# Performance work log

Measured on AMD Instinct MI355X. Metric: run time of the kernel, lower is better.

Reference implementation:

```python
import jax, jax.numpy as jnp
import numpy as np

N, D_MODEL, D_FFN, K = 8192, 1024, 4096, 512


def setup_inputs() -> dict:
    key = jax.random.key(0)
    ks = jax.random.split(key, 5)
    x = jax.random.normal(ks[0], (N, D_MODEL), dtype=jnp.float32)
    topk_indices = jax.random.randint(ks[1], (N, K), 0, D_FFN, dtype=jnp.int32)
    scale = 0.02
    w_gate = jax.random.normal(ks[2], (D_MODEL, D_FFN), dtype=jnp.float32) * scale
    w_up = jax.random.normal(ks[3], (D_MODEL, D_FFN), dtype=jnp.float32) * scale
    w_down = jax.random.normal(ks[4], (D_FFN, D_MODEL), dtype=jnp.float32) * scale
    return {"x": x, "topk_indices": topk_indices, "w_gate": w_gate, "w_up": w_up, "w_down": w_down}


def reference(x, topk_indices, w_gate, w_up, w_down):
    # Dense gate/up projections: [N, d_ffn]
    G = x @ w_gate
    U = x @ w_up
    # Gather only the top-k active neurons per token and fuse SwiGLU there.
    G_act = jnp.take_along_axis(G, topk_indices, axis=1)  # [N, k]
    U_act = jnp.take_along_axis(U, topk_indices, axis=1)  # [N, k]
    Z_active = jax.nn.silu(G_act) * U_act                 # [N, k]
    # Sparse-to-dense down projection: scatter active activations back into
    # the d_ffn axis (zeros elsewhere), then dense matmul with w_down.
    n, k = topk_indices.shape
    rows = jnp.arange(n, dtype=topk_indices.dtype)[:, None]
    Z_dense = jnp.zeros((n, w_down.shape[0]), dtype=Z_active.dtype).at[rows, topk_indices].add(Z_active)
    return Z_dense @ w_down  # [N, d_model]
```

## Files before the change

### kernel.cpp

```cpp
#include <hip/hip_runtime.h>
#include <hip/hip_bf16.h>
#include <cstdint>
#include <cstddef>

#define N_TOK   8192
#define D_MODEL 1024
#define D_FFN   4096
#define K_TOP   512
#define NHALF   2048

typedef __bf16 bf16_t;
typedef __bf16 bf16x8 __attribute__((ext_vector_type(8)));
typedef __bf16 bf16x4 __attribute__((ext_vector_type(4)));
typedef float  f32x4  __attribute__((ext_vector_type(4)));


__global__ void cvt_f32_bf16(const float* __restrict__ in, bf16_t* __restrict__ out, int n4) {
  int i = blockIdx.x * blockDim.x + threadIdx.x;
  if (i < n4) {
    const f32x4 v = ((const f32x4*)in)[i];
    bf16x4 o;
    o[0] = (bf16_t)v[0]; o[1] = (bf16_t)v[1]; o[2] = (bf16_t)v[2]; o[3] = (bf16_t)v[3];
    ((bf16x4*)out)[i] = o;
  }
}

__global__ void transpose_cvt(const float* __restrict__ in, bf16_t* __restrict__ out,
                              int rows, int cols) {
  __shared__ float tile[32][33];
  const int tx = threadIdx.x, ty = threadIdx.y;
  const int x = blockIdx.x * 32 + tx;
#pragma unroll
  for (int i = 0; i < 32; i += 8) {
    int y = blockIdx.y * 32 + ty + i;
    tile[ty + i][tx] = in[(size_t)y * cols + x];
  }
  __syncthreads();
  const int xo = blockIdx.y * 32 + tx;
#pragma unroll
  for (int i = 0; i < 32; i += 8) {
    int yo = blockIdx.x * 32 + ty + i;
    out[(size_t)yo * rows + xo] = (bf16_t)tile[tx][ty + i];
  }
}

#define ROWS_PER_BLK 4
__global__ __launch_bounds__(256) void count_scatter_lds(
    const int* __restrict__ idx, unsigned int* __restrict__ M) {
  __shared__ unsigned int loc[ROWS_PER_BLK * (D_FFN / 8)];
  const int t = threadIdx.x;
  const int r0 = blockIdx.x * ROWS_PER_BLK;

#pragma unroll
  for (int i = 0; i < ROWS_PER_BLK * (D_FFN / 8) / 256; ++i)
    loc[t + i * 256] = 0;
  __syncthreads();

  const int* ip = idx + (size_t)r0 * K_TOP;
#pragma unroll
  for (int i = 0; i < ROWS_PER_BLK * K_TOP / 256; ++i) {
    const int e = t + i * 256;
    const int lr = e >> 9;
    const int j = ip[e];
    atomicAdd(&loc[lr * (D_FFN / 8) + (j >> 3)], 1u << ((j & 7) * 4));
  }
  __syncthreads();

  unsigned int* op = M + (size_t)r0 * (D_FFN / 8);
#pragma unroll
  for (int i = 0; i < ROWS_PER_BLK * (D_FFN / 8) / 256; ++i)
    op[t + i * 256] = loc[t + i * 256];
}


#define BK 32

__device__ __forceinline__ void gload_lds16(const void* g, void* l) {
#if __has_builtin(__builtin_amdgcn_global_load_lds)
  __builtin_amdgcn_global_load_lds((__attribute__((address_space(1))) void*)(g),
                                   (__attribute__((address_space(3))) void*)(l), 16, 0, 0);
#else
  *(bf16x8*)l = *(const bf16x8*)g;
#endif
}

#define BM1 128
#define BN1 128

__global__ __launch_bounds__(512, 4) void gemm_gateup(
    const bf16_t* __restrict__ A,
    const bf16_t* __restrict__ Bg,
    const bf16_t* __restrict__ Bu,
    const unsigned int* __restrict__ cnt,
    bf16_t* __restrict__ Z,
    int n_base)
{
  __shared__ alignas(16) bf16_t As[BM1 * BK];
  __shared__ alignas(16) bf16_t Bgs[BN1 * BK];
  __shared__ alignas(16) bf16_t Bus[BN1 * BK];

  const int m0 = blockIdx.x * BM1;
  const int n0 = blockIdx.y * BN1;
  const int t = threadIdx.x;
  const int lane = t & 63;
  const int w = t >> 6;
  const int wr = w >> 2, wc = w & 3;
  const int l15 = lane & 15;
  const int kk = (lane >> 4) * 8;

  const int rowi = t >> 2;
  const int coli = (t & 3) * 8;
  const bf16_t* pA  = A  + (size_t)(m0 + rowi) * D_MODEL + coli;
  const bf16_t* pBg = Bg + (size_t)(n_base + n0 + rowi) * D_MODEL + coli;
  const bf16_t* pBu = Bu + (size_t)(n_base + n0 + rowi) * D_MODEL + coli;

  f32x4 accg[4][2] = {};
  f32x4 accu[4][2] = {};

  for (int k0 = 0; k0 < D_MODEL; k0 += BK) {
    gload_lds16(pA,  As  + t * 8);
    gload_lds16(pBg, Bgs + t * 8);
    gload_lds16(pBu, Bus + t * 8);
    pA += BK; pBg += BK; pBu += BK;
    __syncthreads();

    bf16x8 af[4], bgf[2], buf[2];
#pragma unroll
    for (int m = 0; m < 4; ++m)
      af[m] = *(const bf16x8*)(As + (wr * 64 + m * 16 + l15) * BK + kk);
#pragma unroll
    for (int n = 0; n < 2; ++n) {
      bgf[n] = *(const bf16x8*)(Bgs + (wc * 32 + n * 16 + l15) * BK + kk);
      buf[n] = *(const bf16x8*)(Bus + (wc * 32 + n * 16 + l15) * BK + kk);
    }
#pragma unroll
    for (int m = 0; m < 4; ++m)
#pragma unroll
      for (int n = 0; n < 2; ++n) {
        accg[m][n] = __builtin_amdgcn_mfma_f32_16x16x32_bf16(af[m], bgf[n], accg[m][n], 0, 0, 0);
        accu[m][n] = __builtin_amdgcn_mfma_f32_16x16x32_bf16(af[m], buf[n], accu[m][n], 0, 0, 0);
      }
    __syncthreads();
  }

#pragma unroll
  for (int m = 0; m < 4; ++m) {
#pragma unroll
    for (int n = 0; n < 2; ++n) {
      const int colL = n0 + wc * 32 + n * 16 + l15;
      const int jg = n_base + colL;
#pragma unroll
      for (int j = 0; j < 4; ++j) {
        const int row = m0 + wr * 64 + m * 16 + (lane >> 4) * 4 + j;
        float g = accg[m][n][j];
        float u = accu[m][n][j];
        unsigned int cw = cnt[(size_t)row * (D_FFN / 8) + (jg >> 3)];
        float c = (float)((cw >> ((jg & 7) * 4)) & 15u);
        float z = c * u * (g / (1.0f + __expf(-g)));
        Z[(size_t)row * NHALF + colL] = (bf16_t)z;
      }
    }
  }
}

#define BM2 64
#define BN2 128

__global__ __launch_bounds__(256, 4) void gemm_down(
    const bf16_t* __restrict__ A,
    const bf16_t* __restrict__ B,
    float* __restrict__ C,
    int k_base, int accum)
{
  __shared__ alignas(16) bf16_t As[BM2 * BK];
  __shared__ alignas(16) bf16_t Bs[BN2 * BK];

  const int m0 = blockIdx.x * BM2;
  const int n0 = blockIdx.y * BN2;
  const int t = threadIdx.x;
  const int lane = t & 63;
  const int w = t >> 6;
  const int wr = w >> 1, wc = w & 1;
  const int l15 = lane & 15;
  const int kk = (lane >> 4) * 8;

  const int rowi = t >> 2;
  const int coli = (t & 3) * 8;
  const bf16_t* pA = A + (size_t)(m0 + rowi) * NHALF + coli;
  const bf16_t* pB = B + (size_t)(n0 + rowi) * D_FFN + k_base + coli;
  const size_t rstepB = (size_t)64 * D_FFN;

  f32x4 acc[2][4] = {};

  for (int k0 = 0; k0 < NHALF; k0 += BK) {
    gload_lds16(pA,          As + t * 8);
    gload_lds16(pB,          Bs + t * 8);
    gload_lds16(pB + rstepB, Bs + (256 + t) * 8);
    pA += BK; pB += BK;
    __syncthreads();

    bf16x8 af[2], bf[4];
#pragma unroll
    for (int m = 0; m < 2; ++m)
      af[m] = *(const bf16x8*)(As + (wr * 32 + m * 16 + l15) * BK + kk);
#pragma unroll
    for (int n = 0; n < 4; ++n)
      bf[n] = *(const bf16x8*)(Bs + (wc * 64 + n * 16 + l15) * BK + kk);
#pragma unroll
    for (int m = 0; m < 2; ++m)
#pragma unroll
      for (int n = 0; n < 4; ++n)
        acc[m][n] = __builtin_amdgcn_mfma_f32_16x16x32_bf16(af[m], bf[n], acc[m][n], 0, 0, 0);
    __syncthreads();
  }

#pragma unroll
  for (int m = 0; m < 2; ++m) {
#pragma unroll
    for (int n = 0; n < 4; ++n) {
      const int col = n0 + wc * 64 + n * 16 + l15;
#pragma unroll
      for (int j = 0; j < 4; ++j) {
        const int row = m0 + wr * 32 + m * 16 + (lane >> 4) * 4 + j;
        const size_t off = (size_t)row * D_MODEL + col;
        float prev = accum ? C[off] : 0.0f;
        C[off] = prev + acc[m][n][j];
      }
    }
  }
}


extern "C" void kernel_launch(void* const* d_in, const int* in_sizes, int n_in,
                              void* d_out, int out_size, void* d_ws, size_t ws_size,
                              hipStream_t stream) {
  const float* x  = (const float*)d_in[0];
  const int*   idx = (const int*)d_in[1];
  const float* wg = (const float*)d_in[2];
  const float* wu = (const float*)d_in[3];
  const float* wd = (const float*)d_in[4];
  float* out = (float*)d_out;

  char* ws = (char*)d_ws;
  const size_t SZ_XB  = (size_t)N_TOK * D_MODEL * 2;
  const size_t SZ_W   = (size_t)D_MODEL * D_FFN * 2;
  const size_t SZ_CNT = (size_t)N_TOK * D_FFN / 2;
  bf16_t* xb  = (bf16_t*)(ws);
  bf16_t* wgT = (bf16_t*)(ws + SZ_XB);
  bf16_t* wuT = (bf16_t*)(ws + SZ_XB + SZ_W);
  bf16_t* wdT = (bf16_t*)(ws + SZ_XB + 2 * SZ_W);
  unsigned int* cnt = (unsigned int*)(ws + SZ_XB + 3 * SZ_W);
  bf16_t* Z   = (bf16_t*)(ws + SZ_XB + 3 * SZ_W + SZ_CNT);

  count_scatter_lds<<<N_TOK / ROWS_PER_BLK, 256, 0, stream>>>(idx, cnt);
  cvt_f32_bf16<<<(N_TOK * D_MODEL / 4 + 255) / 256, 256, 0, stream>>>(x, xb, N_TOK * D_MODEL / 4);
  transpose_cvt<<<dim3(D_FFN / 32, D_MODEL / 32), dim3(32, 8), 0, stream>>>(wg, wgT, D_MODEL, D_FFN);
  transpose_cvt<<<dim3(D_FFN / 32, D_MODEL / 32), dim3(32, 8), 0, stream>>>(wu, wuT, D_MODEL, D_FFN);
  transpose_cvt<<<dim3(D_MODEL / 32, D_FFN / 32), dim3(32, 8), 0, stream>>>(wd, wdT, D_FFN, D_MODEL);

  gemm_gateup<<<dim3(N_TOK / BM1, NHALF / BN1), 512, 0, stream>>>(xb, wgT, wuT, cnt, Z, 0);
  gemm_down<<<dim3(N_TOK / BM2, D_MODEL / BN2), 256, 0, stream>>>(Z, wdT, out, 0, 0);
  gemm_gateup<<<dim3(N_TOK / BM1, NHALF / BN1), 512, 0, stream>>>(xb, wgT, wuT, cnt, Z, NHALF);
  gemm_down<<<dim3(N_TOK / BM2, D_MODEL / BN2), 256, 0, stream>>>(Z, wdT, out, NHALF, 1);
}
```

Before: 311.0 us.

## Rewrite gate/up GEMM with double-buffered LDS, swizzle and phased MFMA schedule

Replaces the gate/up GEMM with a 256x128 tile, BK=64 kernel. It uses 128KB of dynamic LDS split into two ping-pong buffers, with an XOR-swizzled layout to avoid bank conflicts. Each K step is split into four phases that interleave direct-to-LDS global prefetches of the next tile with MFMA groups, and uses s_setprio and explicit barriers to keep the matrix cores busy. The intent is to hide global load latency and raise per-wave MFMA work, at the cost of occupancy (launch bounds 2, large LDS) and more register pressure.

```diff
diff --git a/kernel.cpp b/kernel.cpp
--- a/kernel.cpp
+++ b/kernel.cpp
@@ -73,8 +73,6 @@
 }
 
 
-#define BK 32
-
 __device__ __forceinline__ void gload_lds16(const void* g, void* l) {
 #if __has_builtin(__builtin_amdgcn_global_load_lds)
   __builtin_amdgcn_global_load_lds((__attribute__((address_space(1))) void*)(g),
@@ -84,10 +82,13 @@
 #endif
 }
 
-#define BM1 128
+#define BM1 256
 #define BN1 128
-
-__global__ __launch_bounds__(512, 4) void gemm_gateup(
+#define BK1 64
+#define NT1 (D_MODEL / BK1)
+#define LDSBUF 65536
+
+__global__ __launch_bounds__(512, 2) void gemm_gateup_8p(
     const bf16_t* __restrict__ A,
     const bf16_t* __restrict__ Bg,
     const bf16_t* __restrict__ Bu,
@@ -95,63 +96,135 @@
     bf16_t* __restrict__ Z,
     int n_base)
 {
-  __shared__ alignas(16) bf16_t As[BM1 * BK];
-  __shared__ alignas(16) bf16_t Bgs[BN1 * BK];
-  __shared__ alignas(16) bf16_t Bus[BN1 * BK];
-
-  const int m0 = blockIdx.x * BM1;
-  const int n0 = blockIdx.y * BN1;
+  extern __shared__ char smem[];
   const int t = threadIdx.x;
   const int lane = t & 63;
   const int w = t >> 6;
-  const int wr = w >> 2, wc = w & 3;
+  const int wr = w >> 1;
+  const int wc = w & 1;
   const int l15 = lane & 15;
-  const int kk = (lane >> 4) * 8;
-
-  const int rowi = t >> 2;
-  const int coli = (t & 3) * 8;
-  const bf16_t* pA  = A  + (size_t)(m0 + rowi) * D_MODEL + coli;
-  const bf16_t* pBg = Bg + (size_t)(n_base + n0 + rowi) * D_MODEL + coli;
-  const bf16_t* pBu = Bu + (size_t)(n_base + n0 + rowi) * D_MODEL + coli;
-
-  f32x4 accg[4][2] = {};
-  f32x4 accu[4][2] = {};
-
-  for (int k0 = 0; k0 < D_MODEL; k0 += BK) {
-    gload_lds16(pA,  As  + t * 8);
-    gload_lds16(pBg, Bgs + t * 8);
-    gload_lds16(pBu, Bus + t * 8);
-    pA += BK; pBg += BK; pBu += BK;
-    __syncthreads();
-
-    bf16x8 af[4], bgf[2], buf[2];
-#pragma unroll
-    for (int m = 0; m < 4; ++m)
-      af[m] = *(const bf16x8*)(As + (wr * 64 + m * 16 + l15) * BK + kk);
-#pragma unroll
-    for (int n = 0; n < 2; ++n) {
-      bgf[n] = *(const bf16x8*)(Bgs + (wc * 32 + n * 16 + l15) * BK + kk);
-      buf[n] = *(const bf16x8*)(Bus + (wc * 32 + n * 16 + l15) * BK + kk);
-    }
-#pragma unroll
-    for (int m = 0; m < 4; ++m)
-#pragma unroll
-      for (int n = 0; n < 2; ++n) {
-        accg[m][n] = __builtin_amdgcn_mfma_f32_16x16x32_bf16(af[m], bgf[n], accg[m][n], 0, 0, 0);
-        accu[m][n] = __builtin_amdgcn_mfma_f32_16x16x32_bf16(af[m], buf[n], accu[m][n], 0, 0, 0);
-      }
-    __syncthreads();
+  const int grp = lane >> 4;
+  const int m0 = blockIdx.x * BM1;
+  const int n0 = blockIdx.y * BN1;
+
+  int offA[4], offB[2];
+#pragma unroll
+  for (int c = 0; c < 4; ++c) {
+    const int s = c * 512 + w * 64 + lane;
+    const int r = s >> 3, cb = (s & 7) ^ (r & 7);
+    offA[c] = (m0 + r) * D_MODEL + cb * 8;
+  }
+#pragma unroll
+  for (int c = 0; c < 2; ++c) {
+    const int s = c * 512 + w * 64 + lane;
+    const int r = s >> 3, cb = (s & 7) ^ (r & 7);
+    offB[c] = (n_base + n0 + r) * D_MODEL + cb * 8;
+  }
+  const int dst0 = (w * 64 + lane) * 16;
+
+  const int swz = l15 & 7;
+  const int a_k0 = wr * 8192 + l15 * 128 + ((0 + grp) ^ swz) * 16;
+  const int a_k1 = wr * 8192 + l15 * 128 + ((4 + grp) ^ swz) * 16;
+  const int bg_k0 = 32768 + wc * 8192 + l15 * 128 + ((0 + grp) ^ swz) * 16;
+  const int bg_k1 = 32768 + wc * 8192 + l15 * 128 + ((4 + grp) ^ swz) * 16;
+  const int bu_k0 = bg_k0 + 16384;
+  const int bu_k1 = bg_k1 + 16384;
+
+#pragma unroll
+  for (int c = 0; c < 4; ++c) gload_lds16(A + offA[c], smem + dst0 + c * 8192);
+#pragma unroll
+  for (int c = 0; c < 2; ++c) gload_lds16(Bg + offB[c], smem + 32768 + dst0 + c * 8192);
+#pragma unroll
+  for (int c = 0; c < 2; ++c) gload_lds16(Bu + offB[c], smem + 49152 + dst0 + c * 8192);
+  asm volatile("s_waitcnt vmcnt(0)" ::: "memory");
+  __builtin_amdgcn_s_barrier();
+
+  f32x4 accg[4][4] = {};
+  f32x4 accu[4][4] = {};
+
+#define MFMA16(ACC, AF, BF)                                                      \
+  _Pragma("unroll")                                                              \
+  for (int m = 0; m < 4; ++m)                                                    \
+    _Pragma("unroll")                                                            \
+    for (int n = 0; n < 4; ++n)                                                  \
+      ACC[m][n] = __builtin_amdgcn_mfma_f32_16x16x32_bf16(AF[m], BF[n], ACC[m][n], 0, 0, 0);
+
+#define PHASE_SYNC_PRE()                                                         \
+  __builtin_amdgcn_s_barrier();                                                  \
+  asm volatile("s_waitcnt lgkmcnt(0)" ::: "memory");                             \
+  __builtin_amdgcn_sched_barrier(0);                                             \
+  __builtin_amdgcn_s_setprio(1);
+
+#define PHASE_SYNC_POST()                                                        \
+  __builtin_amdgcn_s_setprio(0);                                                 \
+  __builtin_amdgcn_s_barrier();
+
+  for (int tt = 0; tt < NT1; ++tt) {
+    char* rb = smem + (tt & 1) * LDSBUF;
+    char* wb = smem + ((tt & 1) ^ 1) * LDSBUF;
+    const int kg = (tt + 1) * BK1;
+    const bool st = (tt + 1 < NT1);
+    bf16x8 af[4], bgf[4], buf_[4];
+
+#pragma unroll
+    for (int m = 0; m < 4; ++m) af[m] = *(const bf16x8*)(rb + a_k0 + m * 2048);
+#pragma unroll
+    for (int n = 0; n < 4; ++n) bgf[n] = *(const bf16x8*)(rb + bg_k0 + n * 2048);
+    if (st) {
+      gload_lds16(A + offA[0] + kg, wb + dst0);
+      gload_lds16(A + offA[1] + kg, wb + dst0 + 8192);
+    }
+    PHASE_SYNC_PRE();
+    MFMA16(accg, af, bgf);
+    PHASE_SYNC_POST();
+
+#pragma unroll
+    for (int n = 0; n < 4; ++n) buf_[n] = *(const bf16x8*)(rb + bu_k0 + n * 2048);
+    if (st) {
+      gload_lds16(A + offA[2] + kg, wb + dst0 + 16384);
+      gload_lds16(A + offA[3] + kg, wb + dst0 + 24576);
+    }
+    PHASE_SYNC_PRE();
+    MFMA16(accu, af, buf_);
+    PHASE_SYNC_POST();
+
+#pragma unroll
+    for (int m = 0; m < 4; ++m) af[m] = *(const bf16x8*)(rb + a_k1 + m * 2048);
+#pragma unroll
+    for (int n = 0; n < 4; ++n) bgf[n] = *(const bf16x8*)(rb + bg_k1 + n * 2048);
+    if (st) {
+      gload_lds16(Bg + offB[0] + kg, wb + 32768 + dst0);
+      gload_lds16(Bg + offB[1] + kg, wb + 32768 + dst0 + 8192);
+    }
+    PHASE_SYNC_PRE();
+    MFMA16(accg, af, bgf);
+    PHASE_SYNC_POST();
+
+#pragma unroll
+    for (int n = 0; n < 4; ++n) buf_[n] = *(const bf16x8*)(rb + bu_k1 + n * 2048);
+    if (st) {
+      gload_lds16(Bu + offB[0] + kg, wb + 49152 + dst0);
+      gload_lds16(Bu + offB[1] + kg, wb + 49152 + dst0 + 8192);
+    }
+    __builtin_amdgcn_s_barrier();
+    asm volatile("s_waitcnt lgkmcnt(0)" ::: "memory");
+    __builtin_amdgcn_sched_barrier(0);
+    __builtin_amdgcn_s_setprio(1);
+    MFMA16(accu, af, buf_);
+    __builtin_amdgcn_s_setprio(0);
+    if (st) asm volatile("s_waitcnt vmcnt(0)" ::: "memory");
+    __builtin_amdgcn_s_barrier();
   }
 
 #pragma unroll
   for (int m = 0; m < 4; ++m) {
 #pragma unroll
-    for (int n = 0; n < 2; ++n) {
-      const int colL = n0 + wc * 32 + n * 16 + l15;
+    for (int n = 0; n < 4; ++n) {
+      const int colL = n0 + wc * 64 + n * 16 + l15;
       const int jg = n_base + colL;
 #pragma unroll
       for (int j = 0; j < 4; ++j) {
-        const int row = m0 + wr * 64 + m * 16 + (lane >> 4) * 4 + j;
+        const int row = m0 + wr * 64 + m * 16 + grp * 4 + j;
         float g = accg[m][n][j];
         float u = accu[m][n][j];
         unsigned int cw = cnt[(size_t)row * (D_FFN / 8) + (jg >> 3)];
@@ -161,8 +234,12 @@
       }
     }
   }
-}
-
+#undef MFMA16
+#undef PHASE_SYNC_PRE
+#undef PHASE_SYNC_POST
+}
+
+#define BK 32
 #define BM2 64
 #define BN2 128
 
@@ -252,14 +329,17 @@
   unsigned int* cnt = (unsigned int*)(ws + SZ_XB + 3 * SZ_W);
   bf16_t* Z   = (bf16_t*)(ws + SZ_XB + 3 * SZ_W + SZ_CNT);
 
+  (void)hipFuncSetAttribute((const void*)gemm_gateup_8p,
+                            hipFuncAttributeMaxDynamicSharedMemorySize, 131072);
+
   count_scatter_lds<<<N_TOK / ROWS_PER_BLK, 256, 0, stream>>>(idx, cnt);
   cvt_f32_bf16<<<(N_TOK * D_MODEL / 4 + 255) / 256, 256, 0, stream>>>(x, xb, N_TOK * D_MODEL / 4);
   transpose_cvt<<<dim3(D_FFN / 32, D_MODEL / 32), dim3(32, 8), 0, stream>>>(wg, wgT, D_MODEL, D_FFN);
   transpose_cvt<<<dim3(D_FFN / 32, D_MODEL / 32), dim3(32, 8), 0, stream>>>(wu, wuT, D_MODEL, D_FFN);
   transpose_cvt<<<dim3(D_MODEL / 32, D_FFN / 32), dim3(32, 8), 0, stream>>>(wd, wdT, D_FFN, D_MODEL);
 
-  gemm_gateup<<<dim3(N_TOK / BM1, NHALF / BN1), 512, 0, stream>>>(xb, wgT, wuT, cnt, Z, 0);
+  gemm_gateup_8p<<<dim3(N_TOK / BM1, NHALF / BN1), 512, 131072, stream>>>(xb, wgT, wuT, cnt, Z, 0);
   gemm_down<<<dim3(N_TOK / BM2, D_MODEL / BN2), 256, 0, stream>>>(Z, wdT, out, 0, 0);
-  gemm_gateup<<<dim3(N_TOK / BM1, NHALF / BN1), 512, 0, stream>>>(xb, wgT, wuT, cnt, Z, NHALF);
+  gemm_gateup_8p<<<dim3(N_TOK / BM1, NHALF / BN1), 512, 131072, stream>>>(xb, wgT, wuT, cnt, Z, NHALF);
   gemm_down<<<dim3(N_TOK / BM2, D_MODEL / BN2), 256, 0, stream>>>(Z, wdT, out, NHALF, 1);
 }
```

Result: faster. 298.0 us (-4.2%).
